# Kernel optimization log

Hardware: AMD Instinct MI355X
Metric: run time of the kernel (lower is better)

## Reference

```python
import jax, jax.numpy as jnp
import numpy as np

VOCAB = 32000
PENTA_DIM = 512
DIM = 512
NUM_HEADS = 8
HEAD_DIM = DIM // NUM_HEADS
CANTOR_DEPTH = 8
K_NEIGHBORS = 64  # local_window, adaptive_window=False
BATCH = 2
SEQ = 2048
EPS = 1e-6


def cantor_coords_from_pentachora(pentachora):
    """Vectorized GeometricCantorFingerprinter over [V,5,D] -> [V] coords in [0,1]."""
    V = pentachora.shape[0]
    # pairwise squared distances between the 5 vertices: [V,5,5]
    diff = pentachora[:, :, None, :] - pentachora[:, None, :, :]
    dist_sq = jnp.sum(diff * diff, axis=-1)
    # Cayley-Menger matrix [V,6,6]
    M = jnp.zeros((V, 6, 6), dtype=pentachora.dtype)
    M = M.at[:, 0, 1:].set(1.0)
    M = M.at[:, 1:, 0].set(1.0)
    M = M.at[:, 1:, 1:].set(dist_sq)
    det = jnp.linalg.det(M)
    volume = jnp.sqrt(jnp.clip(-det / 9216.0, 0.0))
    # edge statistics: 10 upper-triangular edges
    iu, ju = np.triu_indices(5, 1)
    edge_len = jnp.sqrt(dist_sq[:, iu, ju])  # [V,10]
    mean_edge = edge_len.mean(axis=-1)
    std_edge = edge_len.std(axis=-1, ddof=1)  # torch.std is unbiased
    # vertex spread: std (ddof=1) of distances to centroid
    centroid = pentachora.mean(axis=1, keepdims=True)
    cd = jnp.linalg.norm(pentachora - centroid, axis=-1)  # [V,5]
    spread = cd.std(axis=-1, ddof=1)
    volume_norm = jax.nn.sigmoid(volume * 10.0)
    edge_ratio = jax.nn.sigmoid(std_edge / (mean_edge + 1e-6))
    spread_norm = jax.nn.sigmoid(spread)
    x = jnp.clip(volume_norm * 0.4 + edge_ratio * 0.3 + spread_norm * 0.3, EPS, 1.0 - EPS)
    bump = (volume_norm + edge_ratio + spread_norm) * 0.01
    cantor_val = jnp.zeros_like(x)
    factor = 0.5
    for _ in range(CANTOR_DEPTH):  # small fixed unroll
        x_scaled = x * 3.0
        digit = jnp.floor(x_scaled)  # x in (0,1) so trunc==floor
        x_frac = x_scaled - digit
        cantor_val = cantor_val + (digit == 2.0).astype(x.dtype) * factor
        x = jnp.clip(x_frac + bump, EPS, 1.0 - EPS)
        factor *= 0.5
    return jnp.clip(cantor_val, 0.0, 1.0)


def setup_inputs() -> dict:
    key = jax.random.key(0)
    ks = jax.random.split(key, 8)
    pentachora = jax.random.normal(ks[0], (VOCAB, 5, PENTA_DIM), dtype=jnp.float32)
    x = jax.random.normal(ks[1], (BATCH, SEQ, DIM), dtype=jnp.float32)
    token_ids = jax.random.randint(ks[2], (SEQ,), 0, VOCAB)
    s = 1.0 / np.sqrt(DIM)
    Wqkv = jax.random.normal(ks[3], (DIM, 3 * DIM), dtype=jnp.float32) * s
    bqkv = jnp.zeros((3 * DIM,), dtype=jnp.float32)
    Wout = jax.random.normal(ks[4], (DIM, DIM), dtype=jnp.float32) * s
    bout = jnp.zeros((DIM,), dtype=jnp.float32)
    return {"pentachora": pentachora, "x": x, "token_ids": token_ids,
            "Wqkv": Wqkv, "bqkv": bqkv, "Wout": Wout, "bout": bout}


def reference(pentachora, x, token_ids, Wqkv, bqkv, Wout, bout):
    coords = cantor_coords_from_pentachora(pentachora)  # [V]
    c = coords[token_ids]  # [S] per-token Cantor coordinates
    # routing: k nearest tokens in 1D Cantor space (smallest |ci - cj|)
    dist = jnp.abs(c[:, None] - c[None, :])  # [S,S]
    _, routes = jax.lax.top_k(-dist, K_NEIGHBORS)  # [S,K]
    B, S, D = x.shape
    qkv = x @ Wqkv + bqkv  # [B,S,3D]
    qkv = qkv.reshape(B, S, 3, NUM_HEADS, HEAD_DIM).transpose(2, 0, 3, 1, 4)
    q, k, v = qkv[0], qkv[1], qkv[2]  # [B,H,S,hd]
    k_g = k[:, :, routes, :]  # [B,H,S,K,hd]
    v_g = v[:, :, routes, :]
    scale = 1.0 / np.sqrt(HEAD_DIM)
    scores = jnp.einsum('bhqd,bhqkd->bhqk', q, k_g) * scale
    attn = jax.nn.softmax(scores, axis=-1)
    out = jnp.einsum('bhqk,bhqkd->bhqd', attn, v_g)  # [B,H,S,hd]
    out = out.transpose(0, 2, 1, 3).reshape(B, S, D)
    return out @ Wout + bout
```

## Files before the change

### kernel.cpp

```cpp
#include <hip/hip_runtime.h>
#include <math.h>


typedef unsigned short u16;
typedef short short8 __attribute__((ext_vector_type(8)));
typedef u16 u16x8 __attribute__((ext_vector_type(8)));
typedef float floatx4 __attribute__((ext_vector_type(4)));

#define NVOCAB 32000
#define NSEQ 2048

__device__ inline float b2f(u16 u){
  union{unsigned int i; float f;} x; x.i = ((unsigned int)u)<<16; return x.f;
}
__device__ inline u16 f2b(float f){
  union{float f; unsigned int u;} x; x.f = f;
  unsigned int u = x.u;
  u += 0x7fffu + ((u >> 16) & 1u);
  return (u16)(u >> 16);
}
__device__ inline double shfl_xor_d(double v, int m){
  union{double d; int i[2];} x; x.d = v;
  x.i[0] = __shfl_xor(x.i[0], m, 64);
  x.i[1] = __shfl_xor(x.i[1], m, 64);
  return x.d;
}

__global__ void detect_kernel(const u16* __restrict__ p, int* __restrict__ flag){
  int lane = threadIdx.x;
  u16 u = p[lane*2];
  int e = (u >> 7) & 0xff;
  bool pass = (e >= 96 && e <= 144);
  unsigned long long m = __ballot(pass);
  if (lane == 0) *flag = (m == ~0ull) ? 1 : 0;
}

__global__ __launch_bounds__(256) void prep_x_kernel(const void* __restrict__ x,
                                                     const int* __restrict__ flagp,
                                                     u16* __restrict__ xb){
  int f = *flagp;
  size_t i = ((size_t)blockIdx.x*256 + threadIdx.x)*8;
  if (f){
    *(u16x8*)(xb+i) = *(const u16x8*)((const u16*)x + i);
  } else {
    const float* xf = (const float*)x + i;
    float4 a = *(const float4*)xf;
    float4 b = *(const float4*)(xf+4);
    u16x8 o;
    o[0]=f2b(a.x); o[1]=f2b(a.y); o[2]=f2b(a.z); o[3]=f2b(a.w);
    o[4]=f2b(b.x); o[5]=f2b(b.y); o[6]=f2b(b.z); o[7]=f2b(b.w);
    *(u16x8*)(xb+i) = o;
  }
}

__global__ __launch_bounds__(256) void transpose_w_kernel(const void* __restrict__ W1,
                                                          const void* __restrict__ W2,
                                                          u16* __restrict__ Wt1,
                                                          u16* __restrict__ Wt2,
                                                          const int* __restrict__ flagp){
  int f = *flagp;
  __shared__ u16 tile[32][33];
  const int K = 512;
  int bx = blockIdx.x, k0 = blockIdx.y*32;
  const void* W; u16* Wt; int N, n0;
  if (bx < 48){ W = W1; Wt = Wt1; N = 1536; n0 = bx*32; }
  else        { W = W2; Wt = Wt2; N = 512;  n0 = (bx-48)*32; }
  int tx = threadIdx.x & 31, ty = threadIdx.x >> 5;
  #pragma unroll
  for (int i=0;i<32;i+=8){
    int k = k0+ty+i, n = n0+tx;
    u16 v = f ? ((const u16*)W)[(size_t)k*N + n]
              : f2b(((const float*)W)[(size_t)k*N + n]);
    tile[ty+i][tx] = v;
  }
  __syncthreads();
  #pragma unroll
  for (int i=0;i<32;i+=8){
    Wt[(size_t)(n0+ty+i)*K + k0+tx] = tile[tx][ty+i];
  }
}

__global__ __launch_bounds__(256) void penta_sums_kernel(const void* __restrict__ penta,
                                                         const int* __restrict__ flagp,
                                                         const int* __restrict__ tok,
                                                         double* __restrict__ sums){
  int f = *flagp;
  int slot = blockIdx.x*4 + (threadIdx.x>>6);
  int w = tok[slot];
  int lane = threadIdx.x & 63;
  float pf[5][8];
  if (f){
    const u16* base = (const u16*)penta + (size_t)w*2560 + lane*8;
    #pragma unroll
    for (int i=0;i<5;i++){
      u16x8 u = *(const u16x8*)(base + i*512);
      #pragma unroll
      for (int j=0;j<8;j++) pf[i][j] = b2f(u[j]);
    }
  } else {
    const float* base = (const float*)penta + (size_t)w*2560 + lane*8;
    #pragma unroll
    for (int i=0;i<5;i++){
      float4 f0 = *(const float4*)(base + i*512);
      float4 f1 = *(const float4*)(base + i*512 + 4);
      pf[i][0]=f0.x; pf[i][1]=f0.y; pf[i][2]=f0.z; pf[i][3]=f0.w;
      pf[i][4]=f1.x; pf[i][5]=f1.y; pf[i][6]=f1.z; pf[i][7]=f1.w;
    }
  }
  double acc[15];
  #pragma unroll
  for (int k=0;k<15;k++) acc[k]=0.0;
  #pragma unroll
  for (int j=0;j<8;j++){
    double p[5];
    #pragma unroll
    for (int i=0;i<5;i++) p[i] = (double)pf[i][j];
    double mean = (p[0]+p[1]+p[2]+p[3]+p[4])*0.2;
    int idx=0;
    #pragma unroll
    for (int a=0;a<5;a++)
      #pragma unroll
      for (int b=a+1;b<5;b++){ double d=p[a]-p[b]; acc[idx++] += d*d; }
    #pragma unroll
    for (int i=0;i<5;i++){ double d=p[i]-mean; acc[10+i] += d*d; }
  }
  #pragma unroll
  for (int k=0;k<15;k++){
    double s = acc[k];
    for (int off=32; off; off>>=1) s += shfl_xor_d(s, off);
    acc[k]=s;
  }
  if (lane==0){
    double* o = sums + (size_t)slot*15;
    #pragma unroll
    for (int k=0;k<15;k++) o[k]=acc[k];
  }
}

__global__ __launch_bounds__(256) void coords_kernel(const double* __restrict__ sums,
                                                     int* __restrict__ ctok){
  int v = blockIdx.x*256 + threadIdx.x;
  if (v >= NSEQ) return;
  const double* s = sums + (size_t)v*15;
  double ds[10], cd2[5];
  #pragma unroll
  for (int k=0;k<10;k++) ds[k]=s[k];
  #pragma unroll
  for (int k=0;k<5;k++) cd2[k]=s[10+k];
  double M[6][6];
  M[0][0]=1.0; M[0][1]=0.0; M[0][2]=ds[0]; M[0][3]=ds[1]; M[0][4]=ds[2]; M[0][5]=ds[3];
  M[1][0]=0.0; M[1][1]=1.0; M[1][2]=1.0;   M[1][3]=1.0;   M[1][4]=1.0;   M[1][5]=1.0;
  M[2][0]=1.0; M[2][1]=ds[0]; M[2][2]=0.0;   M[2][3]=ds[4]; M[2][4]=ds[5]; M[2][5]=ds[6];
  M[3][0]=1.0; M[3][1]=ds[1]; M[3][2]=ds[4]; M[3][3]=0.0;   M[3][4]=ds[7]; M[3][5]=ds[8];
  M[4][0]=1.0; M[4][1]=ds[2]; M[4][2]=ds[5]; M[4][3]=ds[7]; M[4][4]=0.0;   M[4][5]=ds[9];
  M[5][0]=1.0; M[5][1]=ds[3]; M[5][2]=ds[6]; M[5][3]=ds[8]; M[5][4]=ds[9]; M[5][5]=0.0;
  double det=1.0;
  #pragma unroll
  for (int c=0;c<6;c++){
    double pv = M[c][c];
    det *= pv;
    double inv = 1.0/pv;
    #pragma unroll
    for (int r=c+1;r<6;r++){
      double fq = M[r][c]*inv;
      #pragma unroll
      for (int cc=c+1;cc<6;cc++) M[r][cc] -= fq*M[c][cc];
    }
  }
  double volume = sqrt(fmax(det/9216.0, 0.0));
  double vn = 1.0/(1.0+exp(-10.0*volume));
  double me=0.0, e[10];
  #pragma unroll
  for (int k=0;k<10;k++){ e[k]=sqrt(ds[k]); me+=e[k]; }
  me *= 0.1;
  double var=0.0;
  #pragma unroll
  for (int k=0;k<10;k++){ double d=e[k]-me; var+=d*d; }
  double se = sqrt(var/9.0);
  double er = 1.0/(1.0+exp(-(se/(me+1e-6))));
  double mc=0.0, cd[5];
  #pragma unroll
  for (int k=0;k<5;k++){ cd[k]=sqrt(cd2[k]); mc+=cd[k]; }
  mc *= 0.2;
  double v2=0.0;
  #pragma unroll
  for (int k=0;k<5;k++){ double d=cd[k]-mc; v2+=d*d; }
  double sp = sqrt(v2/4.0);
  double sn = 1.0/(1.0+exp(-sp));
  const double EPSd = 1e-6;
  double x = 0.4*vn + 0.3*er + 0.3*sn;
  x = fmin(fmax(x, EPSd), 1.0-EPSd);
  double bump = (vn+er+sn)*0.01;
  double cv=0.0, factor=0.5;
  #pragma unroll
  for (int it=0; it<8; it++){
    double xs = x*3.0;
    double frac = xs - floor(xs);
    if (xs >= 2.0) cv += factor;
    x = fmin(fmax(frac + bump, EPSd), 1.0-EPSd);
    factor *= 0.5;
  }
  cv = fmin(fmax(cv,0.0),1.0);
  ctok[v] = (int)(cv*256.0 + 0.5);
}

__global__ __launch_bounds__(256) void routes_kernel(const int* __restrict__ ctok,
                                                     int* __restrict__ routes){
  __shared__ int cs[NSEQ];
  __shared__ int hist[256];
  __shared__ int scn[256];
  __shared__ int cnts[256];
  __shared__ int params[3];
  int tid = threadIdx.x;
  int q = blockIdx.x;
  for (int j=tid; j<NSEQ; j+=256) cs[j] = ctok[j];
  hist[tid] = 0;
  if (tid==0) params[2]=0;
  __syncthreads();
  int cq = cs[q];
  int base = tid*8;
  int dloc[8];
  #pragma unroll
  for (int i=0;i<8;i++){
    int d = cs[base+i] - cq; d = d<0 ? -d : d;
    dloc[i] = d;
    atomicAdd(&hist[d], 1);
  }
  __syncthreads();
  scn[tid] = hist[tid];
  __syncthreads();
  #pragma unroll
  for (int off=1; off<256; off<<=1){
    int cur = scn[tid];
    int add = (tid>=off) ? scn[tid-off] : 0;
    __syncthreads();
    scn[tid] = cur + add;
    __syncthreads();
  }
  {
    int incl = scn[tid];
    int prev = (tid==0) ? 0 : scn[tid-1];
    if (incl >= 64 && prev < 64){ params[0]=tid; params[1]=64-prev; }
  }
  __syncthreads();
  int T=params[0], need=params[1];
  int ceq=0;
  #pragma unroll
  for (int i=0;i<8;i++) ceq += (dloc[i]==T) ? 1 : 0;
  cnts[tid]=ceq;
  __syncthreads();
  #pragma unroll
  for (int off=1; off<256; off<<=1){
    int cur = cnts[tid];
    int add = (tid>=off) ? cnts[tid-off] : 0;
    __syncthreads();
    cnts[tid] = cur + add;
    __syncthreads();
  }
  int rank = cnts[tid] - ceq;
  int* rq = routes + q*64;
  #pragma unroll
  for (int i=0;i<8;i++){
    int d = dloc[i];
    bool sel = false;
    if (d < T) sel = true;
    else if (d == T){ sel = (rank < need); rank++; }
    if (sel){
      int pos = atomicAdd(&params[2], 1);
      rq[pos] = base + i;
    }
  }
}

template<int C_FOLLOW>
__global__ __launch_bounds__(256) void gemm_direct(const u16* __restrict__ A,
    const u16* __restrict__ Wt, const void* __restrict__ bias, void* __restrict__ Cout,
    const int* __restrict__ flagp, int M, int N, int K)
{
  int f = *flagp;
  bool c_bf16 = C_FOLLOW ? (f==1) : true;
  int tid = threadIdx.x;
  int wv = tid>>6, lane = tid&63, lr = lane&15, lq = lane>>4;
  int m0 = blockIdx.y<<6, n0 = blockIdx.x<<6;
  const u16* Arow = A  + (size_t)(m0 + (wv<<4) + lr)*K + (lq<<3);
  const u16* Wr0  = Wt + (size_t)(n0 + lr)*K + (lq<<3);
  size_t wstep = (size_t)16*K;
  floatx4 acc[4];
  #pragma unroll
  for (int t=0;t<4;t++) acc[t] = (floatx4){0.f,0.f,0.f,0.f};
  #pragma unroll 4
  for (int k0=0;k0<K;k0+=32){
    short8 af = *(const short8*)(Arow + k0);
    #pragma unroll
    for (int t4=0;t4<4;t4++){
      short8 bfv = *(const short8*)(Wr0 + (size_t)t4*wstep + k0);
      acc[t4] = __builtin_amdgcn_mfma_f32_16x16x32_bf16(af, bfv, acc[t4], 0, 0, 0);
    }
  }
  #pragma unroll
  for (int t4=0;t4<4;t4++){
    #pragma unroll
    for (int r=0;r<4;r++){
      int m = m0 + (wv<<4) + (lq<<2) + r;
      int n = n0 + (t4<<4) + lr;
      float bv = f ? b2f(((const u16*)bias)[n]) : ((const float*)bias)[n];
      float val = acc[t4][r] + bv;
      if (c_bf16) ((u16*)Cout)[(size_t)m*N + n] = f2b(val);
      else        ((float*)Cout)[(size_t)m*N + n] = val;
    }
  }
}

__global__ __launch_bounds__(256) void attn_kernel(const u16* __restrict__ qkv,
                                                   const int* __restrict__ routes,
                                                   u16* __restrict__ outa){
  __shared__ float sc[4][8*65];
  __shared__ int rbuf[4][64];
  int tid = threadIdx.x;
  int wv = tid>>6, lane = tid&63;
  int bq = blockIdx.x*4 + wv;
  int b = bq >> 11;
  int q = bq & 2047;
  rbuf[wv][lane] = routes[(q<<6) + lane];
  int h8 = lane>>3;
  const u16* kb = qkv + (size_t)(b<<11)*1536;
  float qv[8];
  {
    u16x8 qraw = *(const u16x8*)(kb + (size_t)q*1536 + lane*8);
    #pragma unroll
    for (int t=0;t<8;t++) qv[t] = b2f(qraw[t]);
  }
  __syncthreads();
  for (int j=0;j<64;j++){
    int rj = rbuf[wv][j];
    u16x8 kraw = *(const u16x8*)(kb + (size_t)rj*1536 + 512 + lane*8);
    float p = 0.f;
    #pragma unroll
    for (int t=0;t<8;t++) p = fmaf(b2f(kraw[t]), qv[t], p);
    p += __shfl_xor(p, 1, 64);
    p += __shfl_xor(p, 2, 64);
    p += __shfl_xor(p, 4, 64);
    if ((lane&7)==0) sc[wv][h8*65 + j] = p * 0.125f;
  }
  __syncthreads();
  {
    int jg = (lane&7)<<3;
    float sv[8];
    float m = -1e30f;
    #pragma unroll
    for (int t=0;t<8;t++){ sv[t] = sc[wv][h8*65 + jg + t]; m = fmaxf(m, sv[t]); }
    m = fmaxf(m, __shfl_xor(m, 1, 64));
    m = fmaxf(m, __shfl_xor(m, 2, 64));
    m = fmaxf(m, __shfl_xor(m, 4, 64));
    float s = 0.f;
    #pragma unroll
    for (int t=0;t<8;t++){ sv[t] = expf(sv[t]-m); s += sv[t]; }
    s += __shfl_xor(s, 1, 64);
    s += __shfl_xor(s, 2, 64);
    s += __shfl_xor(s, 4, 64);
    float inv = 1.f/s;
    #pragma unroll
    for (int t=0;t<8;t++) sc[wv][h8*65 + jg + t] = sv[t]*inv;
  }
  __syncthreads();
  int dg = (lane&7)<<3;
  const u16* vb = kb + 1024 + (h8<<6) + dg;
  float acc8[8];
  #pragma unroll
  for (int t=0;t<8;t++) acc8[t]=0.f;
  for (int j=0;j<64;j++){
    float p = sc[wv][h8*65 + j];
    u16x8 v8 = *(const u16x8*)(vb + (size_t)rbuf[wv][j]*1536);
    #pragma unroll
    for (int t=0;t<8;t++) acc8[t] = fmaf(p, b2f(v8[t]), acc8[t]);
  }
  u16x8 o;
  #pragma unroll
  for (int t=0;t<8;t++) o[t] = f2b(acc8[t]);
  *(u16x8*)(outa + (size_t)bq*512 + (h8<<6) + dg) = o;
}

extern "C" void kernel_launch(void* const* d_in, const int* in_sizes, int n_in,
                              void* d_out, int out_size, void* d_ws, size_t ws_size,
                              hipStream_t stream) {
  const void* penta = d_in[0];
  const void* x     = d_in[1];
  const int*  tok   = (const int*)d_in[2];
  const void* Wqkv  = d_in[3];
  const void* bqkv  = d_in[4];
  const void* Wout  = d_in[5];
  const void* bout  = d_in[6];

  char* ws = (char*)d_ws;
  int*    flag   = (int*)   (ws + 128000);
  int*    ctok   = (int*)   (ws + 131072);
  int*    routes = (int*)   (ws + 139264);
  double* sums   = (double*)(ws + 663552);
  u16*    xb     = (u16*)   (ws + 4503552);
  u16*    Wt1    = (u16*)   (ws + 8697856);
  u16*    Wt2    = (u16*)   (ws + 10270720);
  u16*    qkv    = (u16*)   (ws + 10795008);
  u16*    attn   = (u16*)   (ws + 23377920);

  detect_kernel<<<dim3(1), dim3(64), 0, stream>>>((const u16*)penta, flag);
  prep_x_kernel<<<dim3(1024), dim3(256), 0, stream>>>(x, flag, xb);
  transpose_w_kernel<<<dim3(64,16), dim3(256), 0, stream>>>(Wqkv, Wout, Wt1, Wt2, flag);
  penta_sums_kernel<<<dim3(512), dim3(256), 0, stream>>>(penta, flag, tok, sums);
  coords_kernel<<<dim3(8), dim3(256), 0, stream>>>(sums, ctok);
  routes_kernel<<<dim3(2048), dim3(256), 0, stream>>>(ctok, routes);
  gemm_direct<0><<<dim3(24,64), dim3(256), 0, stream>>>(xb, Wt1, bqkv, (void*)qkv, flag, 4096, 1536, 512);
  attn_kernel<<<dim3(1024), dim3(256), 0, stream>>>(qkv, routes, attn);
  gemm_direct<1><<<dim3(8,64), dim3(256), 0, stream>>>(attn, Wt2, bout, d_out, flag, 4096, 512, 512);
}
```

Baseline: 520.5 us.

## Deduplicate route computation per Cantor bucket and group attention queries by bucket

```diff
diff --git a/kernel.cpp b/kernel.cpp
--- a/kernel.cpp
+++ b/kernel.cpp
@@ -204,15 +204,45 @@
   ctok[v] = (int)(cv*256.0 + 0.5);
 }
 
+__global__ __launch_bounds__(256) void groups_kernel(const int* __restrict__ ctok,
+                                                     int* __restrict__ perm,
+                                                     int* __restrict__ repq){
+  __shared__ int hist[257];
+  __shared__ int repc[257];
+  __shared__ int offs[257];
+  int tid = threadIdx.x;
+  for (int i=tid;i<257;i+=256){ hist[i]=0; repc[i]=0x7fffffff; }
+  __syncthreads();
+  for (int j=tid;j<NSEQ;j+=256){
+    int c = ctok[j];
+    atomicAdd(&hist[c],1);
+    atomicMin(&repc[c], j);
+  }
+  __syncthreads();
+  if (tid==0){
+    int acc=0;
+    for (int i=0;i<257;i++){ offs[i]=acc; acc+=hist[i]; }
+  }
+  __syncthreads();
+  for (int j=tid;j<NSEQ;j+=256){
+    int c = ctok[j];
+    int pos = atomicAdd(&offs[c],1);
+    perm[pos]=j;
+    repq[j]=repc[c];
+  }
+}
+
 __global__ __launch_bounds__(256) void routes_kernel(const int* __restrict__ ctok,
+                                                     const int* __restrict__ repq,
                                                      int* __restrict__ routes){
+  int q = blockIdx.x;
+  if (repq[q] != q) return;
   __shared__ int cs[NSEQ];
   __shared__ int hist[256];
   __shared__ int scn[256];
   __shared__ int cnts[256];
   __shared__ int params[3];
   int tid = threadIdx.x;
-  int q = blockIdx.x;
   for (int j=tid; j<NSEQ; j+=256) cs[j] = ctok[j];
   hist[tid] = 0;
   if (tid==0) params[2]=0;
@@ -313,15 +343,20 @@
 
 __global__ __launch_bounds__(256) void attn_kernel(const u16* __restrict__ qkv,
                                                    const int* __restrict__ routes,
+                                                   const int* __restrict__ perm,
+                                                   const int* __restrict__ repq,
                                                    u16* __restrict__ outa){
   __shared__ float sc[4][8*65];
   __shared__ int rbuf[4][64];
   int tid = threadIdx.x;
   int wv = tid>>6, lane = tid&63;
-  int bq = blockIdx.x*4 + wv;
-  int b = bq >> 11;
-  int q = bq & 2047;
-  rbuf[wv][lane] = routes[(q<<6) + lane];
+  int bid = blockIdx.x;
+  int swz = ((bid&7)<<7) + (bid>>3);
+  int idx = swz*4 + wv;
+  int slot = idx>>1;
+  int b = idx&1;
+  int q = perm[slot];
+  rbuf[wv][lane] = routes[(repq[q]<<6) + lane];
   int h8 = lane>>3;
   const u16* kb = qkv + (size_t)(b<<11)*1536;
   float qv[8];
@@ -377,7 +412,7 @@
   u16x8 o;
   #pragma unroll
   for (int t=0;t<8;t++) o[t] = f2b(acc8[t]);
-  *(u16x8*)(outa + (size_t)bq*512 + (h8<<6) + dg) = o;
+  *(u16x8*)(outa + (size_t)((b<<11)+q)*512 + (h8<<6) + dg) = o;
 }
 
 extern "C" void kernel_launch(void* const* d_in, const int* in_sizes, int n_in,
@@ -396,6 +431,8 @@
   int*    ctok   = (int*)   (ws + 131072);
   int*    routes = (int*)   (ws + 139264);
   double* sums   = (double*)(ws + 663552);
+  int*    perm   = (int*)   (ws + 917504);
+  int*    repq   = (int*)   (ws + 925696);
   u16*    xb     = (u16*)   (ws + 4503552);
   u16*    Wt1    = (u16*)   (ws + 8697856);
   u16*    Wt2    = (u16*)   (ws + 10270720);
@@ -407,8 +444,9 @@
   transpose_w_kernel<<<dim3(64,16), dim3(256), 0, stream>>>(Wqkv, Wout, Wt1, Wt2, flag);
   penta_sums_kernel<<<dim3(512), dim3(256), 0, stream>>>(penta, flag, tok, sums);
   coords_kernel<<<dim3(8), dim3(256), 0, stream>>>(sums, ctok);
-  routes_kernel<<<dim3(2048), dim3(256), 0, stream>>>(ctok, routes);
+  groups_kernel<<<dim3(1), dim3(256), 0, stream>>>(ctok, perm, repq);
+  routes_kernel<<<dim3(2048), dim3(256), 0, stream>>>(ctok, repq, routes);
   gemm_direct<0><<<dim3(24,64), dim3(256), 0, stream>>>(xb, Wt1, bqkv, (void*)qkv, flag, 4096, 1536, 512);
-  attn_kernel<<<dim3(1024), dim3(256), 0, stream>>>(qkv, routes, attn);
+  attn_kernel<<<dim3(1024), dim3(256), 0, stream>>>(qkv, routes, perm, repq, attn);
   gemm_direct<1><<<dim3(8,64), dim3(256), 0, stream>>>(attn, Wt2, bout, d_out, flag, 4096, 512, 512);
 }
```

Result: no change. 526.2 us (+1.1%).

## Fuse prep and coords kernels, inline dtype detection, dedupe route computation per coordinate

Applied to the files above, without the earlier changes.

```diff
diff --git a/kernel.cpp b/kernel.cpp
--- a/kernel.cpp
+++ b/kernel.cpp
@@ -25,43 +25,43 @@
   x.i[1] = __shfl_xor(x.i[1], m, 64);
   return x.d;
 }
-
-__global__ void detect_kernel(const u16* __restrict__ p, int* __restrict__ flag){
-  int lane = threadIdx.x;
+__device__ inline int detect_flag(const u16* __restrict__ p){
+  int lane = threadIdx.x & 63;
   u16 u = p[lane*2];
   int e = (u >> 7) & 0xff;
-  bool pass = (e >= 96 && e <= 144);
-  unsigned long long m = __ballot(pass);
-  if (lane == 0) *flag = (m == ~0ull) ? 1 : 0;
-}
-
-__global__ __launch_bounds__(256) void prep_x_kernel(const void* __restrict__ x,
-                                                     const int* __restrict__ flagp,
-                                                     u16* __restrict__ xb){
-  int f = *flagp;
-  size_t i = ((size_t)blockIdx.x*256 + threadIdx.x)*8;
-  if (f){
-    *(u16x8*)(xb+i) = *(const u16x8*)((const u16*)x + i);
-  } else {
-    const float* xf = (const float*)x + i;
-    float4 a = *(const float4*)xf;
-    float4 b = *(const float4*)(xf+4);
-    u16x8 o;
-    o[0]=f2b(a.x); o[1]=f2b(a.y); o[2]=f2b(a.z); o[3]=f2b(a.w);
-    o[4]=f2b(b.x); o[5]=f2b(b.y); o[6]=f2b(b.z); o[7]=f2b(b.w);
-    *(u16x8*)(xb+i) = o;
-  }
-}
-
-__global__ __launch_bounds__(256) void transpose_w_kernel(const void* __restrict__ W1,
-                                                          const void* __restrict__ W2,
-                                                          u16* __restrict__ Wt1,
-                                                          u16* __restrict__ Wt2,
-                                                          const int* __restrict__ flagp){
-  int f = *flagp;
+  unsigned long long m = __ballot(e >= 96 && e <= 144);
+  return (m == ~0ull) ? 1 : 0;
+}
+
+__global__ __launch_bounds__(256) void prep_kernel(const void* __restrict__ x,
+                                                   const void* __restrict__ W1,
+                                                   const void* __restrict__ W2,
+                                                   const u16* __restrict__ penta,
+                                                   u16* __restrict__ xb,
+                                                   u16* __restrict__ Wt1,
+                                                   u16* __restrict__ Wt2){
+  int f = detect_flag(penta);
+  int bid = blockIdx.x;
+  if (bid < 1024){
+    size_t i = ((size_t)bid*256 + threadIdx.x)*8;
+    if (f){
+      *(u16x8*)(xb+i) = *(const u16x8*)((const u16*)x + i);
+    } else {
+      const float* xf = (const float*)x + i;
+      float4 a = *(const float4*)xf;
+      float4 b = *(const float4*)(xf+4);
+      u16x8 o;
+      o[0]=f2b(a.x); o[1]=f2b(a.y); o[2]=f2b(a.z); o[3]=f2b(a.w);
+      o[4]=f2b(b.x); o[5]=f2b(b.y); o[6]=f2b(b.z); o[7]=f2b(b.w);
+      *(u16x8*)(xb+i) = o;
+    }
+    return;
+  }
+  int idx = bid - 1024;
+  int bx = idx & 63;
+  int k0 = (idx >> 6) * 32;
   __shared__ u16 tile[32][33];
   const int K = 512;
-  int bx = blockIdx.x, k0 = blockIdx.y*32;
   const void* W; u16* Wt; int N, n0;
   if (bx < 48){ W = W1; Wt = Wt1; N = 1536; n0 = bx*32; }
   else        { W = W2; Wt = Wt2; N = 512;  n0 = (bx-48)*32; }
@@ -80,11 +80,10 @@
   }
 }
 
-__global__ __launch_bounds__(256) void penta_sums_kernel(const void* __restrict__ penta,
-                                                         const int* __restrict__ flagp,
-                                                         const int* __restrict__ tok,
-                                                         double* __restrict__ sums){
-  int f = *flagp;
+__global__ __launch_bounds__(256) void penta_coords_kernel(const void* __restrict__ penta,
+                                                           const int* __restrict__ tok,
+                                                           int* __restrict__ ctok){
+  int f = detect_flag((const u16*)penta);
   int slot = blockIdx.x*4 + (threadIdx.x>>6);
   int w = tok[slot];
   int lane = threadIdx.x & 63;
@@ -130,23 +129,12 @@
     for (int off=32; off; off>>=1) s += shfl_xor_d(s, off);
     acc[k]=s;
   }
-  if (lane==0){
-    double* o = sums + (size_t)slot*15;
-    #pragma unroll
-    for (int k=0;k<15;k++) o[k]=acc[k];
-  }
-}
-
-__global__ __launch_bounds__(256) void coords_kernel(const double* __restrict__ sums,
-                                                     int* __restrict__ ctok){
-  int v = blockIdx.x*256 + threadIdx.x;
-  if (v >= NSEQ) return;
-  const double* s = sums + (size_t)v*15;
+  if (lane != 0) return;
   double ds[10], cd2[5];
   #pragma unroll
-  for (int k=0;k<10;k++) ds[k]=s[k];
-  #pragma unroll
-  for (int k=0;k<5;k++) cd2[k]=s[10+k];
+  for (int k=0;k<10;k++) ds[k]=acc[k];
+  #pragma unroll
+  for (int k=0;k<5;k++) cd2[k]=acc[10+k];
   double M[6][6];
   M[0][0]=1.0; M[0][1]=0.0; M[0][2]=ds[0]; M[0][3]=ds[1]; M[0][4]=ds[2]; M[0][5]=ds[3];
   M[1][0]=0.0; M[1][1]=1.0; M[1][2]=1.0;   M[1][3]=1.0;   M[1][4]=1.0;   M[1][5]=1.0;
@@ -201,24 +189,37 @@
     factor *= 0.5;
   }
   cv = fmin(fmax(cv,0.0),1.0);
-  ctok[v] = (int)(cv*256.0 + 0.5);
+  ctok[slot] = (int)(cv*256.0 + 0.5);
 }
 
 __global__ __launch_bounds__(256) void routes_kernel(const int* __restrict__ ctok,
+                                                     int* __restrict__ repq,
                                                      int* __restrict__ routes){
   __shared__ int cs[NSEQ];
   __shared__ int hist[256];
   __shared__ int scn[256];
   __shared__ int cnts[256];
   __shared__ int params[3];
+  __shared__ int repsh;
   int tid = threadIdx.x;
   int q = blockIdx.x;
   for (int j=tid; j<NSEQ; j+=256) cs[j] = ctok[j];
   hist[tid] = 0;
-  if (tid==0) params[2]=0;
+  if (tid==0){ params[2]=0; repsh=0x7fffffff; }
   __syncthreads();
   int cq = cs[q];
   int base = tid*8;
+  {
+    int myrep = 0x7fffffff;
+    #pragma unroll
+    for (int i=0;i<8;i++){
+      if (cs[base+i]==cq && myrep==0x7fffffff) myrep = base+i;
+    }
+    if (myrep != 0x7fffffff) atomicMin(&repsh, myrep);
+  }
+  __syncthreads();
+  if (tid==0) repq[q] = repsh;
+  if (repsh != q) return;
   int dloc[8];
   #pragma unroll
   for (int i=0;i<8;i++){
@@ -275,9 +276,9 @@
 template<int C_FOLLOW>
 __global__ __launch_bounds__(256) void gemm_direct(const u16* __restrict__ A,
     const u16* __restrict__ Wt, const void* __restrict__ bias, void* __restrict__ Cout,
-    const int* __restrict__ flagp, int M, int N, int K)
+    const u16* __restrict__ penta, int M, int N, int K)
 {
-  int f = *flagp;
+  int f = detect_flag(penta);
   bool c_bf16 = C_FOLLOW ? (f==1) : true;
   int tid = threadIdx.x;
   int wv = tid>>6, lane = tid&63, lr = lane&15, lq = lane>>4;
@@ -313,6 +314,7 @@
 
 __global__ __launch_bounds__(256) void attn_kernel(const u16* __restrict__ qkv,
                                                    const int* __restrict__ routes,
+                                                   const int* __restrict__ repq,
                                                    u16* __restrict__ outa){
   __shared__ float sc[4][8*65];
   __shared__ int rbuf[4][64];
@@ -321,7 +323,7 @@
   int bq = blockIdx.x*4 + wv;
   int b = bq >> 11;
   int q = bq & 2047;
-  rbuf[wv][lane] = routes[(q<<6) + lane];
+  rbuf[wv][lane] = routes[(repq[q]<<6) + lane];
   int h8 = lane>>3;
   const u16* kb = qkv + (size_t)(b<<11)*1536;
   float qv[8];
@@ -392,23 +394,19 @@
   const void* bout  = d_in[6];
 
   char* ws = (char*)d_ws;
-  int*    flag   = (int*)   (ws + 128000);
-  int*    ctok   = (int*)   (ws + 131072);
-  int*    routes = (int*)   (ws + 139264);
-  double* sums   = (double*)(ws + 663552);
-  u16*    xb     = (u16*)   (ws + 4503552);
-  u16*    Wt1    = (u16*)   (ws + 8697856);
-  u16*    Wt2    = (u16*)   (ws + 10270720);
-  u16*    qkv    = (u16*)   (ws + 10795008);
-  u16*    attn   = (u16*)   (ws + 23377920);
-
-  detect_kernel<<<dim3(1), dim3(64), 0, stream>>>((const u16*)penta, flag);
-  prep_x_kernel<<<dim3(1024), dim3(256), 0, stream>>>(x, flag, xb);
-  transpose_w_kernel<<<dim3(64,16), dim3(256), 0, stream>>>(Wqkv, Wout, Wt1, Wt2, flag);
-  penta_sums_kernel<<<dim3(512), dim3(256), 0, stream>>>(penta, flag, tok, sums);
-  coords_kernel<<<dim3(8), dim3(256), 0, stream>>>(sums, ctok);
-  routes_kernel<<<dim3(2048), dim3(256), 0, stream>>>(ctok, routes);
-  gemm_direct<0><<<dim3(24,64), dim3(256), 0, stream>>>(xb, Wt1, bqkv, (void*)qkv, flag, 4096, 1536, 512);
-  attn_kernel<<<dim3(1024), dim3(256), 0, stream>>>(qkv, routes, attn);
-  gemm_direct<1><<<dim3(8,64), dim3(256), 0, stream>>>(attn, Wt2, bout, d_out, flag, 4096, 512, 512);
-}
+  int*    ctok   = (int*)   (ws + 0);
+  int*    repq   = (int*)   (ws + 8192);
+  int*    routes = (int*)   (ws + 16384);
+  u16*    xb     = (u16*)   (ws + 1048576);
+  u16*    Wt1    = (u16*)   (ws + 5242880);
+  u16*    Wt2    = (u16*)   (ws + 6815744);
+  u16*    qkv    = (u16*)   (ws + 7340032);
+  u16*    attn   = (u16*)   (ws + 19922944);
+
+  prep_kernel<<<dim3(2048), dim3(256), 0, stream>>>(x, Wqkv, Wout, (const u16*)penta, xb, Wt1, Wt2);
+  penta_coords_kernel<<<dim3(512), dim3(256), 0, stream>>>(penta, tok, ctok);
+  routes_kernel<<<dim3(2048), dim3(256), 0, stream>>>(ctok, repq, routes);
+  gemm_direct<0><<<dim3(24,64), dim3(256), 0, stream>>>(xb, Wt1, bqkv, (void*)qkv, (const u16*)penta, 4096, 1536, 512);
+  attn_kernel<<<dim3(1024), dim3(256), 0, stream>>>(qkv, routes, repq, attn);
+  gemm_direct<1><<<dim3(8,64), dim3(256), 0, stream>>>(attn, Wt2, bout, d_out, (const u16*)penta, 4096, 512, 512);
+}
```

New measurement: 518.0 us. No clear change (-0.5%).
